# Kernel optimization log

Hardware: AMD Instinct MI355X
Metric: run time of the kernel (lower is better)

Reference implementation:

```python
import jax, jax.numpy as jnp
import numpy as np

B, S, D = 2, 2048, 2048
H, KVH, HD = 32, 8, 64
ROPE_THETA = 500000.0


def _rope_cos_sin(seq_len, head_dim, theta, batch):
    inv_freq = 1.0 / (theta ** (jnp.arange(0, head_dim, 2, dtype=jnp.float32) / head_dim))  # [HD/2]
    pos = jnp.arange(seq_len, dtype=jnp.float32)
    freqs = jnp.outer(pos, inv_freq)                      # [S, HD/2]
    emb = jnp.concatenate([freqs, freqs], axis=-1)        # [S, HD]
    cos = jnp.broadcast_to(jnp.cos(emb), (batch, seq_len, head_dim))
    sin = jnp.broadcast_to(jnp.sin(emb), (batch, seq_len, head_dim))
    return cos, sin


def setup_inputs() -> dict:
    key = jax.random.key(0)
    kx, kq, kk, kv, ko = jax.random.split(key, 5)
    x = jax.random.normal(kx, (B, S, D), dtype=jnp.float32)
    cos, sin = _rope_cos_sin(S, HD, ROPE_THETA, B)
    scale = 0.02
    Wq = jax.random.normal(kq, (H * HD, D), dtype=jnp.float32) * scale
    Wk = jax.random.normal(kk, (KVH * HD, D), dtype=jnp.float32) * scale
    Wv = jax.random.normal(kv, (KVH * HD, D), dtype=jnp.float32) * scale
    Wo = jax.random.normal(ko, (D, H * HD), dtype=jnp.float32) * scale
    return {"x": x, "cos": cos, "sin": sin, "Wq": Wq, "Wk": Wk, "Wv": Wv, "Wo": Wo}


def rotate_half(t):
    t1, t2 = jnp.split(t, 2, axis=-1)
    return jnp.concatenate([-t2, t1], axis=-1)


def reference(x, cos, sin, Wq, Wk, Wv, Wo):
    b, s, d = x.shape
    scaling = HD ** -0.5
    groups = H // KVH
    # projections (torch Linear: y = x @ W.T)
    q = jnp.einsum('bsd,od->bso', x, Wq).reshape(b, s, H, HD).transpose(0, 2, 1, 3)    # [B,H,S,HD]
    k = jnp.einsum('bsd,od->bso', x, Wk).reshape(b, s, KVH, HD).transpose(0, 2, 1, 3)  # [B,KVH,S,HD]
    v = jnp.einsum('bsd,od->bso', x, Wv).reshape(b, s, KVH, HD).transpose(0, 2, 1, 3)
    # RoPE (cos/sin unsqueezed over head dim)
    c = cos[:, None, :, :]
    sn = sin[:, None, :, :]
    q = q * c + rotate_half(q) * sn
    k = k * c + rotate_half(k) * sn
    # GQA: repeat kv heads
    k = jnp.repeat(k, groups, axis=1)  # [B,H,S,HD]
    v = jnp.repeat(v, groups, axis=1)
    # causal eager SDPA
    scores = jnp.einsum('bhqd,bhkd->bhqk', q, k) * scaling
    causal = jnp.tril(jnp.ones((s, s), dtype=bool))
    scores = jnp.where(causal[None, None], scores, jnp.finfo(scores.dtype).min)
    attn_weights = jax.nn.softmax(scores, axis=-1)
    attn = jnp.einsum('bhqk,bhkd->bhqd', attn_weights, v)
    attn = attn.transpose(0, 2, 1, 3).reshape(b, s, H * HD)
    out = jnp.einsum('bso,do->bsd', attn, Wo)
    return out
```

## Files before the change

### kernel.cpp

```cpp
#include <hip/hip_runtime.h>
#include <hip/hip_bf16.h>

typedef __attribute__((ext_vector_type(8))) short bf16x8_t;
typedef __attribute__((ext_vector_type(4))) float f32x4;

#define S_LEN  2048
#define NB     2
#define NH     32
#define NKVH   8
#define HD     64
#define DMODEL 2048

__device__ __forceinline__ void gload16(const __hip_bfloat16* g, __hip_bfloat16* l) {
  __builtin_amdgcn_global_load_lds(
      (const __attribute__((address_space(1))) void*)g,
      (__attribute__((address_space(3))) void*)l, 16, 0, 0);
}

__global__ void cvt_kernel(const float* __restrict__ in, __hip_bfloat16* __restrict__ out, int n4) {
  int i = blockIdx.x * blockDim.x + threadIdx.x;
  if (i >= n4) return;
  float4 v = ((const float4*)in)[i];
  __hip_bfloat16 o0 = __float2bfloat16(v.x), o1 = __float2bfloat16(v.y);
  __hip_bfloat16 o2 = __float2bfloat16(v.z), o3 = __float2bfloat16(v.w);
  ushort4 pk;
  pk.x = *(unsigned short*)&o0; pk.y = *(unsigned short*)&o1;
  pk.z = *(unsigned short*)&o2; pk.w = *(unsigned short*)&o3;
  ((ushort4*)out)[i] = pk;
}

__global__ __launch_bounds__(256)
void gemm_qkv(const __hip_bfloat16* __restrict__ A,
              const __hip_bfloat16* __restrict__ Wq,
              const __hip_bfloat16* __restrict__ Wk,
              const __hip_bfloat16* __restrict__ Wv,
              __hip_bfloat16* __restrict__ Qo,
              __hip_bfloat16* __restrict__ Ko,
              __hip_bfloat16* __restrict__ Vto,
              const float* __restrict__ cosb,
              const float* __restrict__ sinb)
{
  __shared__ __align__(16) __hip_bfloat16 As[128][32];
  __shared__ __align__(16) __hip_bfloat16 Bs[128][32];
  const int K = DMODEL;

  const int tid  = threadIdx.x;
  const int lane = tid & 63;
  const int w    = tid >> 6;
  const int wr   = (w >> 1) * 64;
  const int wc   = (w & 1) * 64;
  const int brow = blockIdx.y * 128;
  const int fr   = lane & 15;
  const int fg   = lane >> 4;

  const int bc = blockIdx.x * 128;
  const __hip_bfloat16* Bt; int bcol; int path;
  if (bc < 2048)      { Bt = Wq; bcol = bc;        path = 0; }
  else if (bc < 2560) { Bt = Wk; bcol = bc - 2048; path = 1; }
  else                { Bt = Wv; bcol = bc - 2560; path = 2; }

  const f32x4 fz = {0.f, 0.f, 0.f, 0.f};
  f32x4 acc[4][4];
#pragma unroll
  for (int i = 0; i < 4; ++i)
#pragma unroll
    for (int j = 0; j < 4; ++j) acc[i][j] = fz;

  const int lrow = lane >> 2;
  const int lcol = (lane & 3) * 8;
  const __hip_bfloat16* Ag = A  + (size_t)(brow + w * 32 + lrow) * K + lcol;
  const __hip_bfloat16* Bg = Bt + (size_t)(bcol + w * 32 + lrow) * K + lcol;
  __hip_bfloat16* lA0 = &As[w * 32][0];
  __hip_bfloat16* lA1 = &As[w * 32 + 16][0];
  __hip_bfloat16* lB0 = &Bs[w * 32][0];
  __hip_bfloat16* lB1 = &Bs[w * 32 + 16][0];

  for (int kt = 0; kt < K; kt += 32) {
    __syncthreads();
    gload16(Ag + kt, lA0);
    gload16(Ag + (size_t)16 * K + kt, lA1);
    gload16(Bg + kt, lB0);
    gload16(Bg + (size_t)16 * K + kt, lB1);
    asm volatile("s_waitcnt vmcnt(0)" ::: "memory");
    __syncthreads();

    bf16x8_t af[4], bfr[4];
#pragma unroll
    for (int mi = 0; mi < 4; ++mi)
      af[mi] = *(const bf16x8_t*)&As[wr + mi * 16 + fr][fg * 8];
#pragma unroll
    for (int ni = 0; ni < 4; ++ni)
      bfr[ni] = *(const bf16x8_t*)&Bs[wc + ni * 16 + fr][fg * 8];
#pragma unroll
    for (int mi = 0; mi < 4; ++mi)
#pragma unroll
      for (int ni = 0; ni < 4; ++ni)
        acc[mi][ni] = __builtin_amdgcn_mfma_f32_16x16x32_bf16(af[mi], bfr[ni], acc[mi][ni], 0, 0, 0);
  }

  if (path == 2) {
#pragma unroll
    for (int mi = 0; mi < 4; ++mi) {
#pragma unroll
      for (int ni = 0; ni < 4; ++ni) {
        const int row0 = brow + wr + mi * 16 + fg * 4;
        const int col  = bcol + wc + ni * 16 + fr;
        const int b = row0 >> 11, s = row0 & 2047;
        const int kvh = col >> 6, d = col & 63;
        __hip_bfloat16 v0 = __float2bfloat16(acc[mi][ni][0]);
        __hip_bfloat16 v1 = __float2bfloat16(acc[mi][ni][1]);
        __hip_bfloat16 v2 = __float2bfloat16(acc[mi][ni][2]);
        __hip_bfloat16 v3 = __float2bfloat16(acc[mi][ni][3]);
        ushort4 pk;
        pk.x = *(unsigned short*)&v0; pk.y = *(unsigned short*)&v1;
        pk.z = *(unsigned short*)&v2; pk.w = *(unsigned short*)&v3;
        *(ushort4*)&Vto[(((size_t)b * NKVH + kvh) * HD + d) * S_LEN + s] = pk;
      }
    }
  } else {
    __hip_bfloat16* C = (path == 0) ? Qo : Ko;
    const int N = (path == 0) ? (NH * HD) : (NKVH * HD);
#pragma unroll
    for (int mi = 0; mi < 4; ++mi) {
#pragma unroll
      for (int r = 0; r < 4; ++r) {
        const int row = brow + wr + mi * 16 + fg * 4 + r;
#pragma unroll
        for (int ni = 0; ni < 2; ++ni) {
          const int colL = bcol + wc + ni * 16 + fr;
          const int d    = (colL & 63);
          const float c  = cosb[(size_t)row * HD + d];
          const float sn = sinb[(size_t)row * HD + d];
          const float v0 = acc[mi][ni][r];
          const float v1 = acc[mi][ni + 2][r];
          C[(size_t)row * N + colL]      = __float2bfloat16(v0 * c - v1 * sn);
          C[(size_t)row * N + colL + 32] = __float2bfloat16(v1 * c + v0 * sn);
        }
      }
    }
  }
}

__global__ __launch_bounds__(256)
void gemm_o(const __hip_bfloat16* __restrict__ A,
            const __hip_bfloat16* __restrict__ Bt,
            float* __restrict__ C)
{
  __shared__ __align__(16) __hip_bfloat16 As[128][32];
  __shared__ __align__(16) __hip_bfloat16 Bs[128][32];
  const int K = DMODEL, N = DMODEL;

  const int tid  = threadIdx.x;
  const int lane = tid & 63;
  const int w    = tid >> 6;
  const int wr   = (w >> 1) * 64;
  const int wc   = (w & 1) * 64;
  const int brow = blockIdx.y * 128;
  const int bcol = blockIdx.x * 128;
  const int fr   = lane & 15;
  const int fg   = lane >> 4;

  const f32x4 fz = {0.f, 0.f, 0.f, 0.f};
  f32x4 acc[4][4];
#pragma unroll
  for (int i = 0; i < 4; ++i)
#pragma unroll
    for (int j = 0; j < 4; ++j) acc[i][j] = fz;

  const int lrow = lane >> 2;
  const int lcol = (lane & 3) * 8;
  const __hip_bfloat16* Ag = A  + (size_t)(brow + w * 32 + lrow) * K + lcol;
  const __hip_bfloat16* Bg = Bt + (size_t)(bcol + w * 32 + lrow) * K + lcol;
  __hip_bfloat16* lA0 = &As[w * 32][0];
  __hip_bfloat16* lA1 = &As[w * 32 + 16][0];
  __hip_bfloat16* lB0 = &Bs[w * 32][0];
  __hip_bfloat16* lB1 = &Bs[w * 32 + 16][0];

  for (int kt = 0; kt < K; kt += 32) {
    __syncthreads();
    gload16(Ag + kt, lA0);
    gload16(Ag + (size_t)16 * K + kt, lA1);
    gload16(Bg + kt, lB0);
    gload16(Bg + (size_t)16 * K + kt, lB1);
    asm volatile("s_waitcnt vmcnt(0)" ::: "memory");
    __syncthreads();

    bf16x8_t af[4], bfr[4];
#pragma unroll
    for (int mi = 0; mi < 4; ++mi)
      af[mi] = *(const bf16x8_t*)&As[wr + mi * 16 + fr][fg * 8];
#pragma unroll
    for (int ni = 0; ni < 4; ++ni)
      bfr[ni] = *(const bf16x8_t*)&Bs[wc + ni * 16 + fr][fg * 8];
#pragma unroll
    for (int mi = 0; mi < 4; ++mi)
#pragma unroll
      for (int ni = 0; ni < 4; ++ni)
        acc[mi][ni] = __builtin_amdgcn_mfma_f32_16x16x32_bf16(af[mi], bfr[ni], acc[mi][ni], 0, 0, 0);
  }

#pragma unroll
  for (int mi = 0; mi < 4; ++mi)
#pragma unroll
    for (int ni = 0; ni < 4; ++ni) {
      const int row0 = brow + wr + mi * 16 + fg * 4;
      const int col  = bcol + wc + ni * 16 + fr;
#pragma unroll
      for (int r = 0; r < 4; ++r)
        C[(size_t)(row0 + r) * N + col] = acc[mi][ni][r];
    }
}

__global__ __launch_bounds__(256)
void attn_kernel(const __hip_bfloat16* __restrict__ Q, const __hip_bfloat16* __restrict__ K,
                 const __hip_bfloat16* __restrict__ Vt, __hip_bfloat16* __restrict__ O)
{
  __shared__ __align__(16) __hip_bfloat16 Ks[64][72];
  __shared__ __align__(16) __hip_bfloat16 Vs[64][72];
  __shared__ __align__(16) __hip_bfloat16 Ps[4][16][72];

  const int lane = threadIdx.x & 63;
  const int w    = threadIdx.x >> 6;
  const int fr   = lane & 15;
  const int fg   = lane >> 4;
  const int bh   = blockIdx.y;
  const int b    = bh >> 5;
  const int h    = bh & 31;
  const int kvh  = h >> 2;
  const int qt    = gridDim.x - 1 - blockIdx.x;
  const int qbase = qt * 64;

  const __hip_bfloat16* Qg = Q + ((size_t)(b * S_LEN + qbase)) * DMODEL + h * HD;
  const __hip_bfloat16* Kg = K + (size_t)b * S_LEN * (NKVH * HD) + kvh * HD;
  const __hip_bfloat16* Vg = Vt + ((size_t)(b * NKVH + kvh)) * HD * S_LEN;

  bf16x8_t qf[2];
#pragma unroll
  for (int kk = 0; kk < 2; ++kk)
    qf[kk] = *(const bf16x8_t*)(Qg + (size_t)(w * 16 + fr) * DMODEL + kk * 32 + fg * 8);

  const f32x4 fz = {0.f, 0.f, 0.f, 0.f};
  f32x4 acc[4];
#pragma unroll
  for (int i = 0; i < 4; ++i) acc[i] = fz;
  float m_ = -1e30f, l_ = 0.f;

  const int qrow = qbase + w * 16 + fr;

  const int ktiles = qt + 1;
  for (int t = 0; t < ktiles; ++t) {
    const int kt = t * 64;
    __syncthreads();
    {
      const int r = threadIdx.x >> 2, c = (threadIdx.x & 3) * 16;
      const bf16x8_t* ksrc = (const bf16x8_t*)(Kg + (size_t)(kt + r) * (NKVH * HD) + c);
      *(bf16x8_t*)&Ks[r][c]     = ksrc[0];
      *(bf16x8_t*)&Ks[r][c + 8] = ksrc[1];
      const bf16x8_t* vsrc = (const bf16x8_t*)(Vg + (size_t)r * S_LEN + kt + c);
      *(bf16x8_t*)&Vs[r][c]     = vsrc[0];
      *(bf16x8_t*)&Vs[r][c + 8] = vsrc[1];
    }
    __syncthreads();

    f32x4 sc[4];
#pragma unroll
    for (int c = 0; c < 4; ++c) {
      bf16x8_t k0 = *(const bf16x8_t*)&Ks[c * 16 + fr][fg * 8];
      bf16x8_t k1 = *(const bf16x8_t*)&Ks[c * 16 + fr][32 + fg * 8];
      sc[c] = __builtin_amdgcn_mfma_f32_16x16x32_bf16(k0, qf[0], fz, 0, 0, 0);
      sc[c] = __builtin_amdgcn_mfma_f32_16x16x32_bf16(k1, qf[1], sc[c], 0, 0, 0);
    }

    float p[4][4];
    float tm = -1e30f;
#pragma unroll
    for (int c = 0; c < 4; ++c)
#pragma unroll
      for (int r = 0; r < 4; ++r) {
        float v = sc[c][r] * 0.125f;
        const int kcol = kt + c * 16 + fg * 4 + r;
        if (kcol > qrow) v = -1e30f;
        p[c][r] = v;
        tm = fmaxf(tm, v);
      }
    tm = fmaxf(tm, __shfl_xor(tm, 16));
    tm = fmaxf(tm, __shfl_xor(tm, 32));

    const float mnew = fmaxf(m_, tm);
    const float sf = __expf(m_ - mnew);
    m_ = mnew;

    float ts = 0.f;
#pragma unroll
    for (int c = 0; c < 4; ++c)
#pragma unroll
      for (int r = 0; r < 4; ++r) {
        p[c][r] = __expf(p[c][r] - m_);
        ts += p[c][r];
      }
    ts += __shfl_xor(ts, 16);
    ts += __shfl_xor(ts, 32);
    l_ = l_ * sf + ts;

    float sfv[4];
#pragma unroll
    for (int r = 0; r < 4; ++r) sfv[r] = __shfl(sf, fg * 4 + r);
#pragma unroll
    for (int fc = 0; fc < 4; ++fc)
#pragma unroll
      for (int r = 0; r < 4; ++r) acc[fc][r] *= sfv[r];

#pragma unroll
    for (int c = 0; c < 4; ++c) {
      __hip_bfloat16 b0 = __float2bfloat16(p[c][0]);
      __hip_bfloat16 b1 = __float2bfloat16(p[c][1]);
      __hip_bfloat16 b2 = __float2bfloat16(p[c][2]);
      __hip_bfloat16 b3 = __float2bfloat16(p[c][3]);
      ushort4 pk;
      pk.x = *(unsigned short*)&b0; pk.y = *(unsigned short*)&b1;
      pk.z = *(unsigned short*)&b2; pk.w = *(unsigned short*)&b3;
      *(ushort4*)&Ps[w][fr][c * 16 + fg * 4] = pk;
    }

#pragma unroll
    for (int kk = 0; kk < 2; ++kk) {
      bf16x8_t pa = *(const bf16x8_t*)&Ps[w][fr][kk * 32 + fg * 8];
#pragma unroll
      for (int fc = 0; fc < 4; ++fc) {
        bf16x8_t vf = *(const bf16x8_t*)&Vs[fc * 16 + fr][kk * 32 + fg * 8];
        acc[fc] = __builtin_amdgcn_mfma_f32_16x16x32_bf16(pa, vf, acc[fc], 0, 0, 0);
      }
    }
  }

  float lv[4];
#pragma unroll
  for (int r = 0; r < 4; ++r) lv[r] = __builtin_amdgcn_rcpf(__shfl(l_, fg * 4 + r));
#pragma unroll
  for (int fc = 0; fc < 4; ++fc)
#pragma unroll
    for (int r = 0; r < 4; ++r) {
      const size_t row = (size_t)(b * S_LEN + qbase + w * 16 + fg * 4 + r);
      O[row * DMODEL + h * HD + fc * 16 + fr] = __float2bfloat16(acc[fc][r] * lv[r]);
    }
}

extern "C" void kernel_launch(void* const* d_in, const int* in_sizes, int n_in,
                              void* d_out, int out_size, void* d_ws, size_t ws_size,
                              hipStream_t stream)
{
  const float* x    = (const float*)d_in[0];
  const float* cosb = (const float*)d_in[1];
  const float* sinb = (const float*)d_in[2];
  const float* Wq   = (const float*)d_in[3];
  const float* Wk   = (const float*)d_in[4];
  const float* Wv   = (const float*)d_in[5];
  const float* Wo   = (const float*)d_in[6];
  float* out = (float*)d_out;

  char* p = (char*)d_ws;
  __hip_bfloat16* x_bf    = (__hip_bfloat16*)p; p += (size_t)NB * S_LEN * DMODEL * 2;
  __hip_bfloat16* Wq_bf   = (__hip_bfloat16*)p; p += (size_t)NH * HD * DMODEL * 2;
  __hip_bfloat16* Wk_bf   = (__hip_bfloat16*)p; p += (size_t)NKVH * HD * DMODEL * 2;
  __hip_bfloat16* Wv_bf   = (__hip_bfloat16*)p; p += (size_t)NKVH * HD * DMODEL * 2;
  __hip_bfloat16* Wo_bf   = (__hip_bfloat16*)p; p += (size_t)DMODEL * NH * HD * 2;
  __hip_bfloat16* Q_bf    = (__hip_bfloat16*)p; p += (size_t)NB * S_LEN * NH * HD * 2;
  __hip_bfloat16* K_bf    = (__hip_bfloat16*)p; p += (size_t)NB * S_LEN * NKVH * HD * 2;
  __hip_bfloat16* Vt_bf   = (__hip_bfloat16*)p; p += (size_t)NB * NKVH * HD * S_LEN * 2;
  __hip_bfloat16* attn_bf = (__hip_bfloat16*)p; p += (size_t)NB * S_LEN * NH * HD * 2;

  auto cvt = [&](const float* src, __hip_bfloat16* dst, size_t n) {
    int n4 = (int)(n / 4);
    cvt_kernel<<<(n4 + 255) / 256, 256, 0, stream>>>(src, dst, n4);
  };
  cvt(x,  x_bf,  (size_t)NB * S_LEN * DMODEL);
  cvt(Wq, Wq_bf, (size_t)NH * HD * DMODEL);
  cvt(Wk, Wk_bf, (size_t)NKVH * HD * DMODEL);
  cvt(Wv, Wv_bf, (size_t)NKVH * HD * DMODEL);
  cvt(Wo, Wo_bf, (size_t)DMODEL * NH * HD);

  const dim3 blk(256);
  gemm_qkv<<<dim3(3072 / 128, (NB * S_LEN) / 128), blk, 0, stream>>>(
      x_bf, Wq_bf, Wk_bf, Wv_bf, Q_bf, K_bf, Vt_bf, cosb, sinb);

  attn_kernel<<<dim3(S_LEN / 64, NB * NH), blk, 0, stream>>>(Q_bf, K_bf, Vt_bf, attn_bf);

  gemm_o<<<dim3(DMODEL / 128, (NB * S_LEN) / 128), blk, 0, stream>>>(attn_bf, Wo_bf, out);
}
```

Before: 411.5 us.

## Double-buffer GEMM and attention LDS tiles, widen attention q-tile, fuse conversions

Both GEMM kernels now keep two LDS buffers and prefetch the next K-slice with global_load_lds while the current one feeds MFMA, so each step needs one barrier instead of two. The attention kernel processes 128 query rows per block, with two 16-row sub-tiles per wave sharing K/V fragments. It double-buffers K/V through XOR-swizzled LDS loaded by global_load_lds, and applies the causal mask only on diagonal tiles. The five fp32-to-bf16 conversion launches are merged into one kernel. The cost is more LDS and registers per block, fewer attention blocks, and reliance on the barrier to order the asynchronous LDS loads, since the explicit vmcnt wait was removed.

```diff
diff --git a/kernel.cpp b/kernel.cpp
--- a/kernel.cpp
+++ b/kernel.cpp
@@ -10,6 +10,7 @@
 #define NKVH   8
 #define HD     64
 #define DMODEL 2048
+#define SCALE  0.125f
 
 __device__ __forceinline__ void gload16(const __hip_bfloat16* g, __hip_bfloat16* l) {
   __builtin_amdgcn_global_load_lds(
@@ -17,16 +18,25 @@
       (__attribute__((address_space(3))) void*)l, 16, 0, 0);
 }
 
-__global__ void cvt_kernel(const float* __restrict__ in, __hip_bfloat16* __restrict__ out, int n4) {
+struct CvtSeg { const float* src; __hip_bfloat16* dst; int n4; };
+struct CvtArgs { CvtSeg s[5]; };
+
+__global__ __launch_bounds__(256) void cvt_all(CvtArgs a) {
   int i = blockIdx.x * blockDim.x + threadIdx.x;
-  if (i >= n4) return;
-  float4 v = ((const float4*)in)[i];
-  __hip_bfloat16 o0 = __float2bfloat16(v.x), o1 = __float2bfloat16(v.y);
-  __hip_bfloat16 o2 = __float2bfloat16(v.z), o3 = __float2bfloat16(v.w);
-  ushort4 pk;
-  pk.x = *(unsigned short*)&o0; pk.y = *(unsigned short*)&o1;
-  pk.z = *(unsigned short*)&o2; pk.w = *(unsigned short*)&o3;
-  ((ushort4*)out)[i] = pk;
+#pragma unroll
+  for (int k = 0; k < 5; ++k) {
+    if (i < a.s[k].n4) {
+      float4 v = ((const float4*)a.s[k].src)[i];
+      __hip_bfloat16 o0 = __float2bfloat16(v.x), o1 = __float2bfloat16(v.y);
+      __hip_bfloat16 o2 = __float2bfloat16(v.z), o3 = __float2bfloat16(v.w);
+      ushort4 pk;
+      pk.x = *(unsigned short*)&o0; pk.y = *(unsigned short*)&o1;
+      pk.z = *(unsigned short*)&o2; pk.w = *(unsigned short*)&o3;
+      ((ushort4*)a.s[k].dst)[i] = pk;
+      return;
+    }
+    i -= a.s[k].n4;
+  }
 }
 
 __global__ __launch_bounds__(256)
@@ -40,8 +50,8 @@
               const float* __restrict__ cosb,
               const float* __restrict__ sinb)
 {
-  __shared__ __align__(16) __hip_bfloat16 As[128][32];
-  __shared__ __align__(16) __hip_bfloat16 Bs[128][32];
+  __shared__ __align__(16) __hip_bfloat16 As[2][128][32];
+  __shared__ __align__(16) __hip_bfloat16 Bs[2][128][32];
   const int K = DMODEL;
 
   const int tid  = threadIdx.x;
@@ -70,32 +80,35 @@
   const int lcol = (lane & 3) * 8;
   const __hip_bfloat16* Ag = A  + (size_t)(brow + w * 32 + lrow) * K + lcol;
   const __hip_bfloat16* Bg = Bt + (size_t)(bcol + w * 32 + lrow) * K + lcol;
-  __hip_bfloat16* lA0 = &As[w * 32][0];
-  __hip_bfloat16* lA1 = &As[w * 32 + 16][0];
-  __hip_bfloat16* lB0 = &Bs[w * 32][0];
-  __hip_bfloat16* lB1 = &Bs[w * 32 + 16][0];
-
+
+  auto stage = [&](int buf, int kt) {
+    gload16(Ag + kt,                    &As[buf][w * 32][0]);
+    gload16(Ag + (size_t)16 * K + kt,   &As[buf][w * 32 + 16][0]);
+    gload16(Bg + kt,                    &Bs[buf][w * 32][0]);
+    gload16(Bg + (size_t)16 * K + kt,   &Bs[buf][w * 32 + 16][0]);
+  };
+
+  stage(0, 0);
+  __syncthreads();
+  int cur = 0;
   for (int kt = 0; kt < K; kt += 32) {
-    __syncthreads();
-    gload16(Ag + kt, lA0);
-    gload16(Ag + (size_t)16 * K + kt, lA1);
-    gload16(Bg + kt, lB0);
-    gload16(Bg + (size_t)16 * K + kt, lB1);
-    asm volatile("s_waitcnt vmcnt(0)" ::: "memory");
-    __syncthreads();
+    if (kt + 32 < K) stage(cur ^ 1, kt + 32);
 
     bf16x8_t af[4], bfr[4];
 #pragma unroll
     for (int mi = 0; mi < 4; ++mi)
-      af[mi] = *(const bf16x8_t*)&As[wr + mi * 16 + fr][fg * 8];
+      af[mi] = *(const bf16x8_t*)&As[cur][wr + mi * 16 + fr][fg * 8];
 #pragma unroll
     for (int ni = 0; ni < 4; ++ni)
-      bfr[ni] = *(const bf16x8_t*)&Bs[wc + ni * 16 + fr][fg * 8];
+      bfr[ni] = *(const bf16x8_t*)&Bs[cur][wc + ni * 16 + fr][fg * 8];
 #pragma unroll
     for (int mi = 0; mi < 4; ++mi)
 #pragma unroll
       for (int ni = 0; ni < 4; ++ni)
         acc[mi][ni] = __builtin_amdgcn_mfma_f32_16x16x32_bf16(af[mi], bfr[ni], acc[mi][ni], 0, 0, 0);
+
+    __syncthreads();
+    cur ^= 1;
   }
 
   if (path == 2) {
@@ -146,8 +159,8 @@
             const __hip_bfloat16* __restrict__ Bt,
             float* __restrict__ C)
 {
-  __shared__ __align__(16) __hip_bfloat16 As[128][32];
-  __shared__ __align__(16) __hip_bfloat16 Bs[128][32];
+  __shared__ __align__(16) __hip_bfloat16 As[2][128][32];
+  __shared__ __align__(16) __hip_bfloat16 Bs[2][128][32];
   const int K = DMODEL, N = DMODEL;
 
   const int tid  = threadIdx.x;
@@ -171,32 +184,35 @@
   const int lcol = (lane & 3) * 8;
   const __hip_bfloat16* Ag = A  + (size_t)(brow + w * 32 + lrow) * K + lcol;
   const __hip_bfloat16* Bg = Bt + (size_t)(bcol + w * 32 + lrow) * K + lcol;
-  __hip_bfloat16* lA0 = &As[w * 32][0];
-  __hip_bfloat16* lA1 = &As[w * 32 + 16][0];
-  __hip_bfloat16* lB0 = &Bs[w * 32][0];
-  __hip_bfloat16* lB1 = &Bs[w * 32 + 16][0];
-
+
+  auto stage = [&](int buf, int kt) {
+    gload16(Ag + kt,                  &As[buf][w * 32][0]);
+    gload16(Ag + (size_t)16 * K + kt, &As[buf][w * 32 + 16][0]);
+    gload16(Bg + kt,                  &Bs[buf][w * 32][0]);
+    gload16(Bg + (size_t)16 * K + kt, &Bs[buf][w * 32 + 16][0]);
+  };
+
+  stage(0, 0);
+  __syncthreads();
+  int cur = 0;
   for (int kt = 0; kt < K; kt += 32) {
-    __syncthreads();
-    gload16(Ag + kt, lA0);
-    gload16(Ag + (size_t)16 * K + kt, lA1);
-    gload16(Bg + kt, lB0);
-    gload16(Bg + (size_t)16 * K + kt, lB1);
-    asm volatile("s_waitcnt vmcnt(0)" ::: "memory");
-    __syncthreads();
+    if (kt + 32 < K) stage(cur ^ 1, kt + 32);
 
     bf16x8_t af[4], bfr[4];
 #pragma unroll
     for (int mi = 0; mi < 4; ++mi)
-      af[mi] = *(const bf16x8_t*)&As[wr + mi * 16 + fr][fg * 8];
+      af[mi] = *(const bf16x8_t*)&As[cur][wr + mi * 16 + fr][fg * 8];
 #pragma unroll
     for (int ni = 0; ni < 4; ++ni)
-      bfr[ni] = *(const bf16x8_t*)&Bs[wc + ni * 16 + fr][fg * 8];
+      bfr[ni] = *(const bf16x8_t*)&Bs[cur][wc + ni * 16 + fr][fg * 8];
 #pragma unroll
     for (int mi = 0; mi < 4; ++mi)
 #pragma unroll
       for (int ni = 0; ni < 4; ++ni)
         acc[mi][ni] = __builtin_amdgcn_mfma_f32_16x16x32_bf16(af[mi], bfr[ni], acc[mi][ni], 0, 0, 0);
+
+    __syncthreads();
+    cur ^= 1;
   }
 
 #pragma unroll
@@ -215,134 +231,168 @@
 void attn_kernel(const __hip_bfloat16* __restrict__ Q, const __hip_bfloat16* __restrict__ K,
                  const __hip_bfloat16* __restrict__ Vt, __hip_bfloat16* __restrict__ O)
 {
-  __shared__ __align__(16) __hip_bfloat16 Ks[64][72];
-  __shared__ __align__(16) __hip_bfloat16 Vs[64][72];
-  __shared__ __align__(16) __hip_bfloat16 Ps[4][16][72];
+  __shared__ __align__(16) __hip_bfloat16 Ks[2][64][64];
+  __shared__ __align__(16) __hip_bfloat16 Vs[2][64][64];
+  __shared__ __align__(16) __hip_bfloat16 Ps[4][2][16][72];
 
   const int lane = threadIdx.x & 63;
   const int w    = threadIdx.x >> 6;
   const int fr   = lane & 15;
   const int fg   = lane >> 4;
+  const int r8   = lane >> 3;
+  const int j8   = lane & 7;
   const int bh   = blockIdx.y;
   const int b    = bh >> 5;
   const int h    = bh & 31;
   const int kvh  = h >> 2;
   const int qt    = gridDim.x - 1 - blockIdx.x;
-  const int qbase = qt * 64;
+  const int qbase = qt * 128;
 
   const __hip_bfloat16* Qg = Q + ((size_t)(b * S_LEN + qbase)) * DMODEL + h * HD;
   const __hip_bfloat16* Kg = K + (size_t)b * S_LEN * (NKVH * HD) + kvh * HD;
   const __hip_bfloat16* Vg = Vt + ((size_t)(b * NKVH + kvh)) * HD * S_LEN;
 
-  bf16x8_t qf[2];
-#pragma unroll
-  for (int kk = 0; kk < 2; ++kk)
-    qf[kk] = *(const bf16x8_t*)(Qg + (size_t)(w * 16 + fr) * DMODEL + kk * 32 + fg * 8);
+  bf16x8_t qf[2][2];
+#pragma unroll
+  for (int s = 0; s < 2; ++s)
+#pragma unroll
+    for (int kk = 0; kk < 2; ++kk)
+      qf[s][kk] = *(const bf16x8_t*)(Qg + (size_t)(w * 32 + s * 16 + fr) * DMODEL + kk * 32 + fg * 8);
 
   const f32x4 fz = {0.f, 0.f, 0.f, 0.f};
-  f32x4 acc[4];
-#pragma unroll
-  for (int i = 0; i < 4; ++i) acc[i] = fz;
-  float m_ = -1e30f, l_ = 0.f;
-
-  const int qrow = qbase + w * 16 + fr;
-
-  const int ktiles = qt + 1;
-  for (int t = 0; t < ktiles; ++t) {
+  f32x4 acc[2][4];
+#pragma unroll
+  for (int s = 0; s < 2; ++s)
+#pragma unroll
+    for (int i = 0; i < 4; ++i) acc[s][i] = fz;
+  float m_[2] = {-1e30f, -1e30f}, l_[2] = {0.f, 0.f};
+
+  auto stage = [&](int buf, int kt) {
+#pragma unroll
+    for (int half = 0; half < 2; ++half) {
+      const int row = w * 16 + half * 8 + r8;
+      gload16(Kg + (size_t)(kt + row) * (NKVH * HD) + (j8 ^ r8) * 8, &Ks[buf][w * 16 + half * 8][0]);
+      gload16(Vg + (size_t)row * S_LEN + kt + (j8 ^ r8) * 8,         &Vs[buf][w * 16 + half * 8][0]);
+    }
+  };
+  auto ldK = [&](int buf, int row, int cidx) -> bf16x8_t {
+    return *(const bf16x8_t*)&Ks[buf][row][(cidx ^ (row & 7)) * 8];
+  };
+  auto ldV = [&](int buf, int row, int cidx) -> bf16x8_t {
+    return *(const bf16x8_t*)&Vs[buf][row][(cidx ^ (row & 7)) * 8];
+  };
+
+  stage(0, 0);
+  __syncthreads();
+  int cur = 0;
+  const int NT = 2 * qt + 2;
+  for (int t = 0; t < NT; ++t) {
     const int kt = t * 64;
+    if (t + 1 < NT) stage(cur ^ 1, kt + 64);
+
+    f32x4 sc[2][4];
+#pragma unroll
+    for (int c = 0; c < 4; ++c) {
+      const int krow = c * 16 + fr;
+      bf16x8_t k0 = ldK(cur, krow, fg);
+      bf16x8_t k1 = ldK(cur, krow, 4 + fg);
+      sc[0][c] = __builtin_amdgcn_mfma_f32_16x16x32_bf16(k0, qf[0][0], fz, 0, 0, 0);
+      sc[0][c] = __builtin_amdgcn_mfma_f32_16x16x32_bf16(k1, qf[0][1], sc[0][c], 0, 0, 0);
+      sc[1][c] = __builtin_amdgcn_mfma_f32_16x16x32_bf16(k0, qf[1][0], fz, 0, 0, 0);
+      sc[1][c] = __builtin_amdgcn_mfma_f32_16x16x32_bf16(k1, qf[1][1], sc[1][c], 0, 0, 0);
+    }
+
+#pragma unroll
+    for (int s = 0; s < 2; ++s) {
+      const int base_s = qbase + w * 32 + s * 16;
+      float p[4][4];
+      float tm = -1e30f;
+      if (kt + 63 > base_s) {
+#pragma unroll
+        for (int c = 0; c < 4; ++c)
+#pragma unroll
+          for (int r = 0; r < 4; ++r) {
+            float v = sc[s][c][r] * SCALE;
+            if (kt + c * 16 + fg * 4 + r > base_s + fr) v = -1e30f;
+            p[c][r] = v; tm = fmaxf(tm, v);
+          }
+      } else {
+#pragma unroll
+        for (int c = 0; c < 4; ++c)
+#pragma unroll
+          for (int r = 0; r < 4; ++r) {
+            float v = sc[s][c][r] * SCALE;
+            p[c][r] = v; tm = fmaxf(tm, v);
+          }
+      }
+      tm = fmaxf(tm, __shfl_xor(tm, 16));
+      tm = fmaxf(tm, __shfl_xor(tm, 32));
+
+      const float mnew = fmaxf(m_[s], tm);
+      const float sf = __expf(m_[s] - mnew);
+      m_[s] = mnew;
+
+      float ts = 0.f;
+#pragma unroll
+      for (int c = 0; c < 4; ++c)
+#pragma unroll
+        for (int r = 0; r < 4; ++r) { p[c][r] = __expf(p[c][r] - mnew); ts += p[c][r]; }
+      ts += __shfl_xor(ts, 16);
+      ts += __shfl_xor(ts, 32);
+      l_[s] = l_[s] * sf + ts;
+
+      float sfv[4];
+#pragma unroll
+      for (int r = 0; r < 4; ++r) sfv[r] = __shfl(sf, fg * 4 + r);
+#pragma unroll
+      for (int fc = 0; fc < 4; ++fc)
+#pragma unroll
+        for (int r = 0; r < 4; ++r) acc[s][fc][r] *= sfv[r];
+
+#pragma unroll
+      for (int c = 0; c < 4; ++c) {
+        __hip_bfloat16 b0 = __float2bfloat16(p[c][0]);
+        __hip_bfloat16 b1 = __float2bfloat16(p[c][1]);
+        __hip_bfloat16 b2 = __float2bfloat16(p[c][2]);
+        __hip_bfloat16 b3 = __float2bfloat16(p[c][3]);
+        ushort4 pk;
+        pk.x = *(unsigned short*)&b0; pk.y = *(unsigned short*)&b1;
+        pk.z = *(unsigned short*)&b2; pk.w = *(unsigned short*)&b3;
+        *(ushort4*)&Ps[w][s][fr][c * 16 + fg * 4] = pk;
+      }
+    }
+
+#pragma unroll
+    for (int kk = 0; kk < 2; ++kk) {
+      bf16x8_t pa0 = *(const bf16x8_t*)&Ps[w][0][fr][kk * 32 + fg * 8];
+      bf16x8_t pa1 = *(const bf16x8_t*)&Ps[w][1][fr][kk * 32 + fg * 8];
+#pragma unroll
+      for (int fc = 0; fc < 4; ++fc) {
+        bf16x8_t vf = ldV(cur, fc * 16 + fr, kk * 4 + fg);
+        acc[0][fc] = __builtin_amdgcn_mfma_f32_16x16x32_bf16(pa0, vf, acc[0][fc], 0, 0, 0);
+        acc[1][fc] = __builtin_amdgcn_mfma_f32_16x16x32_bf16(pa1, vf, acc[1][fc], 0, 0, 0);
+      }
+    }
+
     __syncthreads();
-    {
-      const int r = threadIdx.x >> 2, c = (threadIdx.x & 3) * 16;
-      const bf16x8_t* ksrc = (const bf16x8_t*)(Kg + (size_t)(kt + r) * (NKVH * HD) + c);
-      *(bf16x8_t*)&Ks[r][c]     = ksrc[0];
-      *(bf16x8_t*)&Ks[r][c + 8] = ksrc[1];
-      const bf16x8_t* vsrc = (const bf16x8_t*)(Vg + (size_t)r * S_LEN + kt + c);
-      *(bf16x8_t*)&Vs[r][c]     = vsrc[0];
-      *(bf16x8_t*)&Vs[r][c + 8] = vsrc[1];
-    }
-    __syncthreads();
-
-    f32x4 sc[4];
-#pragma unroll
-    for (int c = 0; c < 4; ++c) {
-      bf16x8_t k0 = *(const bf16x8_t*)&Ks[c * 16 + fr][fg * 8];
-      bf16x8_t k1 = *(const bf16x8_t*)&Ks[c * 16 + fr][32 + fg * 8];
-      sc[c] = __builtin_amdgcn_mfma_f32_16x16x32_bf16(k0, qf[0], fz, 0, 0, 0);
-      sc[c] = __builtin_amdgcn_mfma_f32_16x16x32_bf16(k1, qf[1], sc[c], 0, 0, 0);
-    }
-
-    float p[4][4];
-    float tm = -1e30f;
-#pragma unroll
-    for (int c = 0; c < 4; ++c)
+    cur ^= 1;
+  }
+
+  float lv[2][4];
+#pragma unroll
+  for (int s = 0; s < 2; ++s)
+#pragma unroll
+    for (int r = 0; r < 4; ++r)
+      lv[s][r] = __builtin_amdgcn_rcpf(__shfl(l_[s], fg * 4 + r));
+#pragma unroll
+  for (int s = 0; s < 2; ++s)
+#pragma unroll
+    for (int fc = 0; fc < 4; ++fc)
 #pragma unroll
       for (int r = 0; r < 4; ++r) {
-        float v = sc[c][r] * 0.125f;
-        const int kcol = kt + c * 16 + fg * 4 + r;
-        if (kcol > qrow) v = -1e30f;
-        p[c][r] = v;
-        tm = fmaxf(tm, v);
-      }
-    tm = fmaxf(tm, __shfl_xor(tm, 16));
-    tm = fmaxf(tm, __shfl_xor(tm, 32));
-
-    const float mnew = fmaxf(m_, tm);
-    const float sf = __expf(m_ - mnew);
-    m_ = mnew;
-
-    float ts = 0.f;
-#pragma unroll
-    for (int c = 0; c < 4; ++c)
-#pragma unroll
-      for (int r = 0; r < 4; ++r) {
-        p[c][r] = __expf(p[c][r] - m_);
-        ts += p[c][r];
-      }
-    ts += __shfl_xor(ts, 16);
-    ts += __shfl_xor(ts, 32);
-    l_ = l_ * sf + ts;
-
-    float sfv[4];
-#pragma unroll
-    for (int r = 0; r < 4; ++r) sfv[r] = __shfl(sf, fg * 4 + r);
-#pragma unroll
-    for (int fc = 0; fc < 4; ++fc)
-#pragma unroll
-      for (int r = 0; r < 4; ++r) acc[fc][r] *= sfv[r];
-
-#pragma unroll
-    for (int c = 0; c < 4; ++c) {
-      __hip_bfloat16 b0 = __float2bfloat16(p[c][0]);
-      __hip_bfloat16 b1 = __float2bfloat16(p[c][1]);
-      __hip_bfloat16 b2 = __float2bfloat16(p[c][2]);
-      __hip_bfloat16 b3 = __float2bfloat16(p[c][3]);
-      ushort4 pk;
-      pk.x = *(unsigned short*)&b0; pk.y = *(unsigned short*)&b1;
-      pk.z = *(unsigned short*)&b2; pk.w = *(unsigned short*)&b3;
-      *(ushort4*)&Ps[w][fr][c * 16 + fg * 4] = pk;
-    }
-
-#pragma unroll
-    for (int kk = 0; kk < 2; ++kk) {
-      bf16x8_t pa = *(const bf16x8_t*)&Ps[w][fr][kk * 32 + fg * 8];
-#pragma unroll
-      for (int fc = 0; fc < 4; ++fc) {
-        bf16x8_t vf = *(const bf16x8_t*)&Vs[fc * 16 + fr][kk * 32 + fg * 8];
-        acc[fc] = __builtin_amdgcn_mfma_f32_16x16x32_bf16(pa, vf, acc[fc], 0, 0, 0);
-      }
-    }
-  }
-
-  float lv[4];
-#pragma unroll
-  for (int r = 0; r < 4; ++r) lv[r] = __builtin_amdgcn_rcpf(__shfl(l_, fg * 4 + r));
-#pragma unroll
-  for (int fc = 0; fc < 4; ++fc)
-#pragma unroll
-    for (int r = 0; r < 4; ++r) {
-      const size_t row = (size_t)(b * S_LEN + qbase + w * 16 + fg * 4 + r);
-      O[row * DMODEL + h * HD + fc * 16 + fr] = __float2bfloat16(acc[fc][r] * lv[r]);
-    }
+        const size_t row = (size_t)(b * S_LEN + qbase + w * 32 + s * 16 + fg * 4 + r);
+        O[row * DMODEL + h * HD + fc * 16 + fr] = __float2bfloat16(acc[s][fc][r] * lv[s][r]);
+      }
 }
 
 extern "C" void kernel_launch(void* const* d_in, const int* in_sizes, int n_in,
@@ -369,21 +419,20 @@
   __hip_bfloat16* Vt_bf   = (__hip_bfloat16*)p; p += (size_t)NB * NKVH * HD * S_LEN * 2;
   __hip_bfloat16* attn_bf = (__hip_bfloat16*)p; p += (size_t)NB * S_LEN * NH * HD * 2;
 
-  auto cvt = [&](const float* src, __hip_bfloat16* dst, size_t n) {
-    int n4 = (int)(n / 4);
-    cvt_kernel<<<(n4 + 255) / 256, 256, 0, stream>>>(src, dst, n4);
-  };
-  cvt(x,  x_bf,  (size_t)NB * S_LEN * DMODEL);
-  cvt(Wq, Wq_bf, (size_t)NH * HD * DMODEL);
-  cvt(Wk, Wk_bf, (size_t)NKVH * HD * DMODEL);
-  cvt(Wv, Wv_bf, (size_t)NKVH * HD * DMODEL);
-  cvt(Wo, Wo_bf, (size_t)DMODEL * NH * HD);
+  CvtArgs ca;
+  ca.s[0] = { x,  x_bf,  (int)((size_t)NB * S_LEN * DMODEL / 4) };
+  ca.s[1] = { Wq, Wq_bf, (int)((size_t)NH * HD * DMODEL / 4) };
+  ca.s[2] = { Wk, Wk_bf, (int)((size_t)NKVH * HD * DMODEL / 4) };
+  ca.s[3] = { Wv, Wv_bf, (int)((size_t)NKVH * HD * DMODEL / 4) };
+  ca.s[4] = { Wo, Wo_bf, (int)((size_t)DMODEL * NH * HD / 4) };
+  int total4 = ca.s[0].n4 + ca.s[1].n4 + ca.s[2].n4 + ca.s[3].n4 + ca.s[4].n4;
+  cvt_all<<<(total4 + 255) / 256, 256, 0, stream>>>(ca);
 
   const dim3 blk(256);
   gemm_qkv<<<dim3(3072 / 128, (NB * S_LEN) / 128), blk, 0, stream>>>(
       x_bf, Wq_bf, Wk_bf, Wv_bf, Q_bf, K_bf, Vt_bf, cosb, sinb);
 
-  attn_kernel<<<dim3(S_LEN / 64, NB * NH), blk, 0, stream>>>(Q_bf, K_bf, Vt_bf, attn_bf);
+  attn_kernel<<<dim3(S_LEN / 128, NB * NH), blk, 0, stream>>>(Q_bf, K_bf, Vt_bf, attn_bf);
 
   gemm_o<<<dim3(DMODEL / 128, (NB * S_LEN) / 128), blk, 0, stream>>>(attn_bf, Wo_bf, out);
 }
```

Result: no change. 410.9 us (-0.1%).
